# Optimization experiments

Measured on AMD Instinct MI355X. Metric: run time of the kernel, lower is better.

Reference implementation:

```python
import jax, jax.numpy as jnp
import numpy as np

LENS = 0.4
DECAY = 0.2
THRESH = 0.2
LOG_SIG_MIN, LOG_SIG_MAX = -20.0, 2.0

# Surrogate-gradient spike: forward is heaviside, backward is rectangular window |x|<lens
@jax.custom_vjp
def act_fun(x):
    return (x > 0.0).astype(x.dtype)

def _act_fwd(x):
    return act_fun(x), x

def _act_bwd(x, g):
    return (g * (jnp.abs(x) < LENS).astype(g.dtype),)

act_fun.defvjp(_act_fwd, _act_bwd)


def _xavier(k, shape):
    fan_out, fan_in = shape
    lim = float(np.sqrt(6.0 / (fan_in + fan_out)))
    return jax.random.uniform(k, shape, jnp.float32, -lim, lim)


def setup_inputs() -> dict:
    key = jax.random.key(0)
    ks = jax.random.split(key, 9)
    B, IN, H, A = 4096, 512, 2048, 32
    return {
        "state": jax.random.normal(ks[0], (B, 5, IN), jnp.float32),
        "W_lif": _xavier(ks[1], (H, IN)), "b_lif": jnp.zeros((H,), jnp.float32),
        "W11": _xavier(ks[2], (H, H)), "b11": jnp.zeros((H,), jnp.float32),
        "W12": _xavier(ks[3], (H, H)), "b12": jnp.zeros((H,), jnp.float32),
        "W21": _xavier(ks[4], (H, H)), "b21": jnp.zeros((H,), jnp.float32),
        "W22": _xavier(ks[5], (H, H)), "b22": jnp.zeros((H,), jnp.float32),
        "Wm": _xavier(ks[6], (A, H)), "bm": jnp.zeros((A,), jnp.float32),
        "Wls": _xavier(ks[7], (A, H)), "bls": jnp.zeros((A,), jnp.float32),
    }


def reference(state, W_lif, b_lif, W11, b11, W12, b12, W21, b21, W22, b22, Wm, bm, Wls, bls):
    x_seq = jnp.repeat(state, 3, axis=1)
    # precompute fc(x) for all steps in one GEMM: [B,15,H]
    fc = jnp.einsum('bti,hi->bth', x_seq, W_lif) + b_lif
    B, T, H = fc.shape

    def step(carry, fc_t):
        mem, spike = carry
        mem1 = mem * DECAY * (1.0 - spike) + fc_t
        spike1 = act_fun(mem1 - THRESH)
        return (mem1, spike1), spike1

    init = (jnp.zeros((B, H), fc.dtype), jnp.zeros((B, H), fc.dtype))
    _, spikes = jax.lax.scan(step, init, jnp.swapaxes(fc, 0, 1))  # [T,B,H]
    x = jnp.mean(spikes, axis=0)  # [B,H]

    x1 = jax.nn.relu(x @ W11.T + b11)
    x1 = jax.nn.relu(x1 @ W12.T + b12)
    mean = x1 @ Wm.T + bm

    x2 = jax.nn.relu(x @ W21.T + b21)
    x2 = jax.nn.relu(x2 @ W22.T + b22)
    log_std = jnp.clip(x2 @ Wls.T + bls, LOG_SIG_MIN, LOG_SIG_MAX)
    return mean, log_std
```

## Files before the change

kernel.cpp:

```cpp
#include <hip/hip_runtime.h>
#include <hip/hip_bf16.h>


typedef _Float16 f16;
using f32x4 = __attribute__((ext_vector_type(4))) float;
using f16x8 = __attribute__((ext_vector_type(8))) f16;

#define MFMA16(a, b, c) __builtin_amdgcn_mfma_f32_16x16x32_f16((a), (b), (c), 0, 0, 0)
#define VMW8()  asm volatile("s_waitcnt vmcnt(8)" ::: "memory")
#define VMW0()  asm volatile("s_waitcnt vmcnt(0)" ::: "memory")
#define LGKM0() asm volatile("s_waitcnt lgkmcnt(0)" ::: "memory")
#define BARRIER() __builtin_amdgcn_s_barrier()
#define SCHED0() __builtin_amdgcn_sched_barrier(0)

__device__ __forceinline__ void gload16(const void* g, void* l) {
  __builtin_amdgcn_global_load_lds(
      (const __attribute__((address_space(1))) unsigned int*)g,
      (__attribute__((address_space(3))) unsigned int*)l, 16, 0, 0);
}

__global__ __launch_bounds__(256) void cvt_kernel(
    const float* __restrict__ src, f16* __restrict__ dst, int n8)
{
  int i = blockIdx.x * 256 + threadIdx.x;
  if (i >= n8) return;
  const float4* s4 = (const float4*)src;
  float4 a = s4[(size_t)i * 2], b = s4[(size_t)i * 2 + 1];
  f16x8 d;
  d[0] = (f16)a.x; d[1] = (f16)a.y; d[2] = (f16)a.z; d[3] = (f16)a.w;
  d[4] = (f16)b.x; d[5] = (f16)b.y; d[6] = (f16)b.z; d[7] = (f16)b.w;
  *(f16x8*)(dst + (size_t)i * 8) = d;
}

__global__ __launch_bounds__(256) void cvt2_kernel(
    const float* __restrict__ s0, const float* __restrict__ s1,
    f16* __restrict__ d0, f16* __restrict__ d1, int n8each)
{
  int i = blockIdx.x * 256 + threadIdx.x;
  const float* src = (i < n8each) ? s0 : s1;
  f16* dst = (i < n8each) ? d0 : d1;
  int k = (i < n8each) ? i : i - n8each;
  if (k >= n8each) return;
  const float4* s4 = (const float4*)src;
  float4 a = s4[(size_t)k * 2], b = s4[(size_t)k * 2 + 1];
  f16x8 d;
  d[0] = (f16)a.x; d[1] = (f16)a.y; d[2] = (f16)a.z; d[3] = (f16)a.w;
  d[4] = (f16)b.x; d[5] = (f16)b.y; d[6] = (f16)b.z; d[7] = (f16)b.w;
  *(f16x8*)(dst + (size_t)k * 8) = d;
}

__global__ __launch_bounds__(256) void lif_kernel(
    const f16* __restrict__ S,
    const f16* __restrict__ W,
    const float* __restrict__ bl,
    f16* __restrict__ X)
{
  const int K = 512, N = 2048;
  __shared__ alignas(16) f16 As[2][5][64 * 32];
  __shared__ alignas(16) f16 Bs[2][128 * 32];

  const int tid = threadIdx.x, wid = tid >> 6, lane = tid & 63;
  const int nwg = 1024, q = nwg / 8;
  const int wg = (blockIdx.x % 8) * q + blockIdx.x / 8;
  const int bm = wg % 64, bn = wg / 64;
  const int b0 = bm * 64, h0 = bn * 128;
  const int wr = (wid >> 1) * 32, wc = (wid & 1) * 64;
  const int srow = tid >> 2, skol = (tid & 3) * 8;
  const int kb = (lane >> 4) * 8, fr = lane & 15, fq = lane >> 4;

  f32x4 acc[5][2][4] = {};

  auto STAGE = [&](int p, int k0) {
#pragma unroll
    for (int s = 0; s < 5; ++s)
      gload16(S + ((size_t)(b0 + srow) * 5 + s) * K + k0 + skol, &As[p][s][tid * 8]);
#pragma unroll
    for (int r = 0; r < 2; ++r)
      gload16(W + (size_t)(h0 + r * 64 + srow) * K + k0 + skol, &Bs[p][r * 2048 + tid * 8]);
  };

  STAGE(0, 0);
  __syncthreads();
  int cur = 0;
  for (int kt = 0; kt < 16; ++kt) {
    if (kt + 1 < 16) STAGE(cur ^ 1, (kt + 1) * 32);
    f16x8 bf[4];
#pragma unroll
    for (int n = 0; n < 4; ++n)
      bf[n] = *(const f16x8*)&Bs[cur][(wc + n * 16 + fr) * 32 + kb];
#pragma unroll
    for (int s = 0; s < 5; ++s) {
      f16x8 af[2];
#pragma unroll
      for (int m = 0; m < 2; ++m)
        af[m] = *(const f16x8*)&As[cur][s][(wr + m * 16 + fr) * 32 + kb];
#pragma unroll
      for (int m = 0; m < 2; ++m)
#pragma unroll
        for (int n = 0; n < 4; ++n)
          acc[s][m][n] = MFMA16(af[m], bf[n], acc[s][m][n]);
    }
    __syncthreads();
    cur ^= 1;
  }

#pragma unroll
  for (int m = 0; m < 2; ++m) {
#pragma unroll
    for (int n = 0; n < 4; ++n) {
      const int col = h0 + wc + n * 16 + fr;
      const float bv = bl[col];
#pragma unroll
      for (int r = 0; r < 4; ++r) {
        const int row = b0 + wr + m * 16 + fq * 4 + r;
        float mem = 0.f, spk = 0.f, cnt = 0.f;
#pragma unroll
        for (int s = 0; s < 5; ++s) {
          const float fc = acc[s][m][n][r] + bv;
#pragma unroll
          for (int j = 0; j < 3; ++j) {
            mem = mem * 0.2f * (1.f - spk) + fc;
            spk = (mem > 0.2f) ? 1.f : 0.f;
            cnt += spk;
          }
        }
        X[(size_t)row * N + col] = (f16)(cnt / 15.0f);
      }
    }
  }
}

__global__ __launch_bounds__(512, 2) void trunk256_kernel(
    const f16* __restrict__ A0, const f16* __restrict__ A1, int lda,
    const f16* __restrict__ W0, const f16* __restrict__ W1,
    const float* __restrict__ bb0, const float* __restrict__ bb1,
    f16* __restrict__ C0, f16* __restrict__ C1, int ldc,
    int nbm, int nbn_half, int K)
{
  __shared__ alignas(16) f16 lds[4][256 * 64];

  const int tid = threadIdx.x, wid = tid >> 6, lane = tid & 63;
  const int nwg = nbm * nbn_half * 2, q8 = nwg / 8;
  const int wg = ((int)blockIdx.x % 8) * q8 + (int)blockIdx.x / 8;
  const int bmi = wg % nbm, t = wg / nbm;
  const int half = (t >= nbn_half);
  const f16* Ap = half ? A1 : A0;
  const f16* Wp = half ? W1 : W0;
  const float* bias = half ? bb1 : bb0;
  f16* C = half ? C1 : C0;
  const int bm0 = bmi * 256;
  const int bn0 = (half ? t - nbn_half : t) * 256;

  const int wr0 = (wid >> 2) * 128, wc0 = (wid & 3) * 64;
  const int fr = lane & 15, fq = lane >> 4;
  const int sr = tid >> 3, scb = (tid & 7) * 16;

  f32x4 acc[8][4] = {};
  const int NT = K / 64;

  auto STAGE = [&](int slot, int kt) {
    const int k0 = kt * 64;
#pragma unroll
    for (int l = 0; l < 4; ++l) {
      const int row = l * 64 + sr;
      const int c2 = scb ^ ((row & 7) << 4);
      gload16(Ap + (size_t)(bm0 + row) * lda + k0 + (c2 >> 1),
              &lds[slot][l * 4096 + tid * 8]);
    }
#pragma unroll
    for (int l = 0; l < 4; ++l) {
      const int row = l * 64 + sr;
      const int c2 = scb ^ ((row & 7) << 4);
      gload16(Wp + (size_t)(bn0 + row) * K + k0 + (c2 >> 1),
              &lds[2 + slot][l * 4096 + tid * 8]);
    }
  };

  auto LDA_ = [&](int slot, int mf, int ks) -> f16x8 {
    const int row = wr0 + mf * 16 + fr;
    const int c = (ks * 64 + fq * 16) ^ ((row & 7) << 4);
    return *(const f16x8*)&lds[slot][row * 64 + (c >> 1)];
  };
  auto LDB_ = [&](int slot, int nf, int ks) -> f16x8 {
    const int row = wc0 + nf * 16 + fr;
    const int c = (ks * 64 + fq * 16) ^ ((row & 7) << 4);
    return *(const f16x8*)&lds[2 + slot][row * 64 + (c >> 1)];
  };

  STAGE(0, 0);
  STAGE(1, 1);
  VMW8();
  BARRIER();
  SCHED0();

  for (int kt = 0; kt < NT; ++kt) {
    const int slot = kt & 1;

    f16x8 b[4][2];
#pragma unroll
    for (int nf = 0; nf < 4; ++nf) {
      b[nf][0] = LDB_(slot, nf, 0);
      b[nf][1] = LDB_(slot, nf, 1);
    }
    f16x8 a0[2][2], a1[2][2];
#pragma unroll
    for (int i = 0; i < 2; ++i) {
      a0[i][0] = LDA_(slot, i, 0);
      a0[i][1] = LDA_(slot, i, 1);
    }

    auto QUAD = [&](int mbase, f16x8 (&a)[2][2]) {
      __builtin_amdgcn_s_setprio(1);
#pragma unroll
      for (int nf = 0; nf < 4; ++nf) {
        acc[mbase][nf]     = MFMA16(a[0][0], b[nf][0], acc[mbase][nf]);
        acc[mbase][nf]     = MFMA16(a[0][1], b[nf][1], acc[mbase][nf]);
        acc[mbase + 1][nf] = MFMA16(a[1][0], b[nf][0], acc[mbase + 1][nf]);
        acc[mbase + 1][nf] = MFMA16(a[1][1], b[nf][1], acc[mbase + 1][nf]);
      }
      __builtin_amdgcn_s_setprio(0);
    };

#pragma unroll
    for (int i = 0; i < 2; ++i) { a1[i][0] = LDA_(slot, 2 + i, 0); a1[i][1] = LDA_(slot, 2 + i, 1); }
    QUAD(0, a0);
#pragma unroll
    for (int i = 0; i < 2; ++i) { a0[i][0] = LDA_(slot, 4 + i, 0); a0[i][1] = LDA_(slot, 4 + i, 1); }
    QUAD(2, a1);
#pragma unroll
    for (int i = 0; i < 2; ++i) { a1[i][0] = LDA_(slot, 6 + i, 0); a1[i][1] = LDA_(slot, 6 + i, 1); }
    QUAD(4, a0);
    QUAD(6, a1);

    LGKM0();
    BARRIER();
    SCHED0();
    if (kt + 2 < NT) {
      STAGE(slot, kt + 2);
      SCHED0();
      VMW8();
    } else if (kt + 1 < NT) {
      VMW0();
    }
    BARRIER();
    SCHED0();
  }

#pragma unroll
  for (int nf = 0; nf < 4; ++nf) {
    const int col = bn0 + wc0 + nf * 16 + fr;
    const float bv = bias[col];
#pragma unroll
    for (int m = 0; m < 8; ++m) {
      const int row0 = bm0 + wr0 + m * 16 + fq * 4;
#pragma unroll
      for (int r = 0; r < 4; ++r) {
        float v = fmaxf(acc[m][nf][r] + bv, 0.f);
        C[(size_t)(row0 + r) * ldc + col] = (f16)v;
      }
    }
  }
}

__global__ __launch_bounds__(256) void head_kernel(
    const f16* __restrict__ H1, const f16* __restrict__ H2,
    const f16* __restrict__ Wm, const float* __restrict__ bm,
    const f16* __restrict__ Wls, const float* __restrict__ bls,
    float* __restrict__ OUT, int M, int K)
{
  const int tid = threadIdx.x, wid = tid >> 6, lane = tid & 63;
  const int m0 = blockIdx.x * 64 + wid * 16;
  const int kb = (lane >> 4) * 8, fr = lane & 15, fq = lane >> 4;

  f32x4 a1[2] = {}, a2[2] = {};
  for (int k0 = 0; k0 < K; k0 += 32) {
    f16x8 f1 = *(const f16x8*)&H1[(size_t)(m0 + fr) * K + k0 + kb];
    f16x8 f2 = *(const f16x8*)&H2[(size_t)(m0 + fr) * K + k0 + kb];
#pragma unroll
    for (int n = 0; n < 2; ++n) {
      f16x8 wm = *(const f16x8*)&Wm[(size_t)(n * 16 + fr) * K + k0 + kb];
      f16x8 wl = *(const f16x8*)&Wls[(size_t)(n * 16 + fr) * K + k0 + kb];
      a1[n] = MFMA16(f1, wm, a1[n]);
      a2[n] = MFMA16(f2, wl, a2[n]);
    }
  }

#pragma unroll
  for (int n = 0; n < 2; ++n) {
    const int col = n * 16 + fr;
    const float bvm = bm[col];
    const float bvl = bls[col];
#pragma unroll
    for (int r = 0; r < 4; ++r) {
      const int row = m0 + fq * 4 + r;
      OUT[(size_t)row * 32 + col] = a1[n][r] + bvm;
      float lv = a2[n][r] + bvl;
      OUT[(size_t)M * 32 + (size_t)row * 32 + col] = fminf(fmaxf(lv, -20.f), 2.f);
    }
  }
}

extern "C" void kernel_launch(void* const* d_in, const int* in_sizes, int n_in,
                              void* d_out, int out_size, void* d_ws, size_t ws_size,
                              hipStream_t stream) {
  const float* state = (const float*)d_in[0];
  const float* W_lif = (const float*)d_in[1];
  const float* b_lif = (const float*)d_in[2];
  const float* W11   = (const float*)d_in[3];
  const float* b11   = (const float*)d_in[4];
  const float* W12   = (const float*)d_in[5];
  const float* b12   = (const float*)d_in[6];
  const float* W21   = (const float*)d_in[7];
  const float* b21   = (const float*)d_in[8];
  const float* W22   = (const float*)d_in[9];
  const float* b22   = (const float*)d_in[10];
  const float* Wm    = (const float*)d_in[11];
  const float* bm    = (const float*)d_in[12];
  const float* Wls   = (const float*)d_in[13];
  const float* bls   = (const float*)d_in[14];
  float* out = (float*)d_out;

  const int B = 4096, IN = 512, H = 2048;
  char* ws = (char*)d_ws;
  f16* x    = (f16*)(ws);
  f16* h1   = (f16*)(ws + 16777216);
  f16* h2   = (f16*)(ws + 33554432);
  f16* s16  = (f16*)(ws + 50331648);
  f16* wl16 = (f16*)(ws + 71303168);
  f16* w11h = (f16*)(ws + 50331648);
  f16* w21h = (f16*)(ws + 58720256);
  f16* h22  = (f16*)(ws + 50331648);
  f16* w12h = (f16*)(ws + 67108864);
  f16* w22h = (f16*)(ws + 75497472);
  f16* wmh  = (f16*)(ws + 67108864);
  f16* wlsh = (f16*)(ws + 67239936);
  f16* h12  = x;

  cvt_kernel<<<(B * 5 * IN / 8) / 256, 256, 0, stream>>>(state, s16, B * 5 * IN / 8);
  cvt_kernel<<<(H * IN / 8) / 256, 256, 0, stream>>>(W_lif, wl16, H * IN / 8);

  lif_kernel<<<1024, 256, 0, stream>>>(s16, wl16, b_lif, x);

  cvt2_kernel<<<2 * (H * H / 8) / 256, 256, 0, stream>>>(W11, W21, w11h, w21h, H * H / 8);
  trunk256_kernel<<<256, 512, 0, stream>>>(x, x, H, w11h, w21h, b11, b21,
                                           h1, h2, H, 16, 8, H);

  cvt2_kernel<<<2 * (H * H / 8) / 256, 256, 0, stream>>>(W12, W22, w12h, w22h, H * H / 8);
  trunk256_kernel<<<256, 512, 0, stream>>>(h1, h2, H, w12h, w22h, b12, b22,
                                           h12, h22, H, 16, 8, H);

  cvt2_kernel<<<2 * (32 * H / 8) / 256, 256, 0, stream>>>(Wm, Wls, wmh, wlsh, 32 * H / 8);
  head_kernel<<<B / 64, 256, 0, stream>>>(h12, h22, wmh, bm, wlsh, bls, out, B, H);
}
```

Baseline: 295.8 us.

## Restructure LIF GEMM into 128x128 tiles with timestep-outer K loop and swizzled LDS

Replaces the LIF kernel with a 512-thread, 128x128-tile version that walks the five timesteps sequentially over K, so only one accumulator set per fragment is live instead of five. At each timestep boundary it folds the accumulator into the running membrane and spike-count state. It also adds XOR-swizzled LDS layouts with BK=64, double buffering with vmcnt-based waits, and raised MFMA priority. The aim is lower register pressure, better tile reuse and fewer bank conflicts, at the cost of more barriers per K step.

```diff
diff --git a/kernel.cpp b/kernel.cpp
--- a/kernel.cpp
+++ b/kernel.cpp
@@ -8,6 +8,7 @@
 
 #define MFMA16(a, b, c) __builtin_amdgcn_mfma_f32_16x16x32_f16((a), (b), (c), 0, 0, 0)
 #define VMW8()  asm volatile("s_waitcnt vmcnt(8)" ::: "memory")
+#define VMW4()  asm volatile("s_waitcnt vmcnt(4)" ::: "memory")
 #define VMW0()  asm volatile("s_waitcnt vmcnt(0)" ::: "memory")
 #define LGKM0() asm volatile("s_waitcnt lgkmcnt(0)" ::: "memory")
 #define BARRIER() __builtin_amdgcn_s_barrier()
@@ -49,83 +50,131 @@
   *(f16x8*)(dst + (size_t)k * 8) = d;
 }
 
-__global__ __launch_bounds__(256) void lif_kernel(
+__global__ __launch_bounds__(512, 1) void lif256_kernel(
     const f16* __restrict__ S,
     const f16* __restrict__ W,
     const float* __restrict__ bl,
     f16* __restrict__ X)
 {
-  const int K = 512, N = 2048;
-  __shared__ alignas(16) f16 As[2][5][64 * 32];
-  __shared__ alignas(16) f16 Bs[2][128 * 32];
+  __shared__ alignas(16) f16 lds[4][128 * 64];
 
   const int tid = threadIdx.x, wid = tid >> 6, lane = tid & 63;
-  const int nwg = 1024, q = nwg / 8;
-  const int wg = (blockIdx.x % 8) * q + blockIdx.x / 8;
-  const int bm = wg % 64, bn = wg / 64;
-  const int b0 = bm * 64, h0 = bn * 128;
-  const int wr = (wid >> 1) * 32, wc = (wid & 1) * 64;
-  const int srow = tid >> 2, skol = (tid & 3) * 8;
-  const int kb = (lane >> 4) * 8, fr = lane & 15, fq = lane >> 4;
-
-  f32x4 acc[5][2][4] = {};
-
-  auto STAGE = [&](int p, int k0) {
-#pragma unroll
-    for (int s = 0; s < 5; ++s)
-      gload16(S + ((size_t)(b0 + srow) * 5 + s) * K + k0 + skol, &As[p][s][tid * 8]);
-#pragma unroll
-    for (int r = 0; r < 2; ++r)
-      gload16(W + (size_t)(h0 + r * 64 + srow) * K + k0 + skol, &Bs[p][r * 2048 + tid * 8]);
-  };
+  const int wg = ((int)blockIdx.x % 8) * 64 + (int)blockIdx.x / 8;
+  const int bn = wg & 15, bm = wg >> 4;
+  const int b0 = bm * 128, h0 = bn * 128;
+  const int wr0 = (wid >> 2) * 64, wc0 = (wid & 3) * 32;
+  const int fr = lane & 15, fq = lane >> 4;
+  const int sr = tid >> 3, scb = (tid & 7) * 16;
+
+  f32x4 acc[4][2] = {};
+  float mem[4][2][4] = {};
+  float cnt[4][2][4] = {};
+
+  auto STAGE = [&](int slot, int g) {
+    const int s = g >> 3, k0 = (g & 7) * 64;
+#pragma unroll
+    for (int l = 0; l < 2; ++l) {
+      const int row = l * 64 + sr;
+      const int c2 = scb ^ ((row & 7) << 4);
+      gload16(S + ((size_t)(b0 + row) * 5 + s) * 512 + k0 + (c2 >> 1),
+              &lds[slot][l * 4096 + tid * 8]);
+    }
+#pragma unroll
+    for (int l = 0; l < 2; ++l) {
+      const int row = l * 64 + sr;
+      const int c2 = scb ^ ((row & 7) << 4);
+      gload16(W + (size_t)(h0 + row) * 512 + k0 + (c2 >> 1),
+              &lds[2 + slot][l * 4096 + tid * 8]);
+    }
+  };
+
+  auto LDA_ = [&](int slot, int mf, int ks) -> f16x8 {
+    const int row = wr0 + mf * 16 + fr;
+    const int c = (ks * 64 + fq * 16) ^ ((row & 7) << 4);
+    return *(const f16x8*)&lds[slot][row * 64 + (c >> 1)];
+  };
+  auto LDB_ = [&](int slot, int nf, int ks) -> f16x8 {
+    const int row = wc0 + nf * 16 + fr;
+    const int c = (ks * 64 + fq * 16) ^ ((row & 7) << 4);
+    return *(const f16x8*)&lds[2 + slot][row * 64 + (c >> 1)];
+  };
+
+  const float bias[2] = { bl[h0 + wc0 + fr], bl[h0 + wc0 + 16 + fr] };
 
   STAGE(0, 0);
-  __syncthreads();
-  int cur = 0;
-  for (int kt = 0; kt < 16; ++kt) {
-    if (kt + 1 < 16) STAGE(cur ^ 1, (kt + 1) * 32);
-    f16x8 bf[4];
-#pragma unroll
-    for (int n = 0; n < 4; ++n)
-      bf[n] = *(const f16x8*)&Bs[cur][(wc + n * 16 + fr) * 32 + kb];
-#pragma unroll
-    for (int s = 0; s < 5; ++s) {
-      f16x8 af[2];
-#pragma unroll
-      for (int m = 0; m < 2; ++m)
-        af[m] = *(const f16x8*)&As[cur][s][(wr + m * 16 + fr) * 32 + kb];
-#pragma unroll
-      for (int m = 0; m < 2; ++m)
-#pragma unroll
-        for (int n = 0; n < 4; ++n)
-          acc[s][m][n] = MFMA16(af[m], bf[n], acc[s][m][n]);
-    }
-    __syncthreads();
-    cur ^= 1;
-  }
-
-#pragma unroll
-  for (int m = 0; m < 2; ++m) {
-#pragma unroll
-    for (int n = 0; n < 4; ++n) {
-      const int col = h0 + wc + n * 16 + fr;
-      const float bv = bl[col];
-#pragma unroll
-      for (int r = 0; r < 4; ++r) {
-        const int row = b0 + wr + m * 16 + fq * 4 + r;
-        float mem = 0.f, spk = 0.f, cnt = 0.f;
-#pragma unroll
-        for (int s = 0; s < 5; ++s) {
-          const float fc = acc[s][m][n][r] + bv;
-#pragma unroll
-          for (int j = 0; j < 3; ++j) {
-            mem = mem * 0.2f * (1.f - spk) + fc;
-            spk = (mem > 0.2f) ? 1.f : 0.f;
-            cnt += spk;
+  STAGE(1, 1);
+  VMW4();
+  BARRIER();
+  SCHED0();
+
+  for (int g = 0; g < 40; ++g) {
+    const int slot = g & 1;
+
+    f16x8 b[2][2], a[4][2];
+#pragma unroll
+    for (int nf = 0; nf < 2; ++nf) {
+      b[nf][0] = LDB_(slot, nf, 0);
+      b[nf][1] = LDB_(slot, nf, 1);
+    }
+#pragma unroll
+    for (int mf = 0; mf < 4; ++mf) {
+      a[mf][0] = LDA_(slot, mf, 0);
+      a[mf][1] = LDA_(slot, mf, 1);
+    }
+
+    __builtin_amdgcn_s_setprio(1);
+#pragma unroll
+    for (int mf = 0; mf < 4; ++mf)
+#pragma unroll
+      for (int nf = 0; nf < 2; ++nf) {
+        acc[mf][nf] = MFMA16(a[mf][0], b[nf][0], acc[mf][nf]);
+        acc[mf][nf] = MFMA16(a[mf][1], b[nf][1], acc[mf][nf]);
+      }
+    __builtin_amdgcn_s_setprio(0);
+
+    if ((g & 7) == 7) {
+#pragma unroll
+      for (int mf = 0; mf < 4; ++mf)
+#pragma unroll
+        for (int nf = 0; nf < 2; ++nf) {
+#pragma unroll
+          for (int r = 0; r < 4; ++r) {
+            const float fc = acc[mf][nf][r] + bias[nf];
+            float m = mem[mf][nf][r], c = cnt[mf][nf][r];
+#pragma unroll
+            for (int j = 0; j < 3; ++j) {
+              m = ((m > 0.2f) ? 0.f : m * 0.2f) + fc;
+              c += (m > 0.2f) ? 1.f : 0.f;
+            }
+            mem[mf][nf][r] = m; cnt[mf][nf][r] = c;
           }
+          acc[mf][nf] = f32x4{0.f, 0.f, 0.f, 0.f};
         }
-        X[(size_t)row * N + col] = (f16)(cnt / 15.0f);
-      }
+    }
+
+    LGKM0();
+    BARRIER();
+    SCHED0();
+    if (g + 2 < 40) {
+      STAGE(slot, g + 2);
+      SCHED0();
+      VMW4();
+    } else if (g + 1 < 40) {
+      VMW0();
+    }
+    BARRIER();
+    SCHED0();
+  }
+
+#pragma unroll
+  for (int nf = 0; nf < 2; ++nf) {
+    const int col = h0 + wc0 + nf * 16 + fr;
+#pragma unroll
+    for (int mf = 0; mf < 4; ++mf) {
+      const int row0 = b0 + wr0 + mf * 16 + fq * 4;
+#pragma unroll
+      for (int r = 0; r < 4; ++r)
+        X[(size_t)(row0 + r) * 2048 + col] = (f16)(cnt[mf][nf][r] / 15.0f);
     }
   }
 }
@@ -339,7 +388,7 @@
   cvt_kernel<<<(B * 5 * IN / 8) / 256, 256, 0, stream>>>(state, s16, B * 5 * IN / 8);
   cvt_kernel<<<(H * IN / 8) / 256, 256, 0, stream>>>(W_lif, wl16, H * IN / 8);
 
-  lif_kernel<<<1024, 256, 0, stream>>>(s16, wl16, b_lif, x);
+  lif256_kernel<<<512, 512, 0, stream>>>(s16, wl16, b_lif, x);
 
   cvt2_kernel<<<2 * (H * H / 8) / 256, 256, 0, stream>>>(W11, W21, w11h, w21h, H * H / 8);
   trunk256_kernel<<<256, 512, 0, stream>>>(x, x, H, w11h, w21h, b11, b21,
```

Result: faster. 285.0 us (-3.6%).
